# Optimization experiments

Hardware: AMD Instinct MI355X
Metric: run time of the kernel (lower is better)

## Reference

```python
import jax, jax.numpy as jnp
import numpy as np

B, N, C = 8, 4096, 1024
H = 16
D = C // H  # head_dim = 64
SCALE = D ** -0.5


def setup_inputs() -> dict:
    key = jax.random.key(0)
    ks = jax.random.split(key, 5)
    s = 0.02
    return {
        "x": jax.random.normal(ks[0], (B, N, C), dtype=jnp.float32),
        "Wq": jax.random.normal(ks[1], (C, C), dtype=jnp.float32) * s,
        "Wk": jax.random.normal(ks[2], (C, C), dtype=jnp.float32) * s,
        "Wv": jax.random.normal(ks[3], (C, C), dtype=jnp.float32) * s,
        "Wp": jax.random.normal(ks[4], (C, C), dtype=jnp.float32) * s,
        "bp": jnp.zeros((C,), dtype=jnp.float32),
    }


def reference(x, Wq, Wk, Wv, Wp, bp):
    b, n, c = x.shape
    # nn.Linear: y = x @ W^T (no bias for q/k/v)
    def split_heads(y):
        # (B,N,C) -> (B,N,H,D) -> permute(0,2,3,1) -> (B,H,D,N)
        return jnp.transpose(y.reshape(b, n, H, D), (0, 2, 3, 1))

    q = split_heads(x @ Wq.T)  # (B,H,D,N)
    k = split_heads(x @ Wk.T)  # (B,H,D,N)
    v = split_heads(x @ Wv.T)  # (B,H,D,N)

    # attn over head_dim (faithful to source layout): (B,H,D,D)
    attn = jnp.einsum('bhdn,bhen->bhde', q, k) * SCALE
    attn = jax.nn.softmax(attn, axis=-1)
    # (B,H,D,D) @ (B,H,D,N) -> (B,H,D,N); transpose(1,2) -> (B,D,H,N); reshape (B,N,C)
    out = jnp.einsum('bhde,bhen->bhdn', attn, v)
    out = jnp.transpose(out, (0, 2, 1, 3)).reshape(b, n, c)
    return out @ Wp.T + bp
```

## Files before the change

kernel.cpp:

```cpp
#include <hip/hip_runtime.h>


typedef __attribute__((ext_vector_type(4))) float f32x4;
typedef __attribute__((ext_vector_type(8))) _Float16 f16x8;
typedef __attribute__((ext_vector_type(4))) unsigned short u16x4;

__device__ __forceinline__ unsigned short f2h(float f) {
  union { _Float16 h; unsigned short u; } v;
  v.h = (_Float16)f;
  return v.u;
}

__global__ void cvt_f32_f16(const float* __restrict__ in, unsigned short* __restrict__ out, int n) {
  int i = (blockIdx.x * blockDim.x + threadIdx.x) * 4;
  if (i >= n) return;
  float4 v = *(const float4*)(in + i);
  u16x4 o;
  o.x = f2h(v.x); o.y = f2h(v.y); o.z = f2h(v.z); o.w = f2h(v.w);
  *(u16x4*)(out + i) = o;
}

#define LDS_LD 68
enum { EPI_F16_N = 0, EPI_F16_T = 1, EPI_F32_BIAS = 2 };

template <int EPI>
__global__ __launch_bounds__(256, 2) void gemm_bt(const unsigned short* __restrict__ A,
                                                  const unsigned short* __restrict__ Bt,
                                                  void* __restrict__ Cv,
                                                  const float* __restrict__ bias,
                                                  const int M, const int N, const int K) {
  __shared__ unsigned short lds[4 * 64 * LDS_LD];
  const int tid = threadIdx.x;
  const int wave = tid >> 6, lane = tid & 63;
  const int quad = lane >> 4, l15 = lane & 15;
  const int m0 = blockIdx.y * 128, n0 = blockIdx.x * 128;
  const int mb = (wave & 1) * 64, nb = (wave >> 1) * 64;

  const int sr = lane >> 2;
  const int sc = (lane & 3) ^ ((sr >> 1) & 3);

  const int swz = quad ^ ((l15 >> 1) & 3);
  int a_off[4], b_off[4];
#pragma unroll
  for (int t = 0; t < 4; t++) {
    a_off[t] = ((mb >> 4) + t) * 512 + (l15 * 4 + swz) * 8;
    b_off[t] = 4096 + ((nb >> 4) + t) * 512 + (l15 * 4 + swz) * 8;
  }

  const unsigned short* Ag = A + (size_t)(m0 + sr) * K + sc * 8;
  const unsigned short* Bg = Bt + (size_t)(n0 + sr) * K + sc * 8;

  f32x4 acc[4][4];
#pragma unroll
  for (int i = 0; i < 4; i++)
#pragma unroll
    for (int j = 0; j < 4; j++) acc[i][j] = f32x4{0.f, 0.f, 0.f, 0.f};

  for (int k0 = 0; k0 < K; k0 += 32) {
    __syncthreads();
#pragma unroll
    for (int rd = 0; rd < 2; rd++) {
      const int ch = rd * 4 + wave;
      __builtin_amdgcn_global_load_lds(
          (const __attribute__((address_space(1))) void*)(Ag + (size_t)ch * 16 * K + k0),
          (__attribute__((address_space(3))) void*)&lds[ch * 512], 16, 0, 0);
      __builtin_amdgcn_global_load_lds(
          (const __attribute__((address_space(1))) void*)(Bg + (size_t)ch * 16 * K + k0),
          (__attribute__((address_space(3))) void*)&lds[4096 + ch * 512], 16, 0, 0);
    }
    __syncthreads();

    f16x8 af[4], bf[4];
#pragma unroll
    for (int t = 0; t < 4; t++) {
      af[t] = *(const f16x8*)&lds[a_off[t]];
      bf[t] = *(const f16x8*)&lds[b_off[t]];
    }
#pragma unroll
    for (int mi = 0; mi < 4; mi++)
#pragma unroll
      for (int ni = 0; ni < 4; ni++)
        acc[mi][ni] = __builtin_amdgcn_mfma_f32_16x16x32_f16(af[mi], bf[ni], acc[mi][ni], 0, 0, 0);
  }

  __syncthreads();

  if (EPI == EPI_F32_BIAS) {
    float* C = (float*)Cv;
#pragma unroll
    for (int ni = 0; ni < 4; ni++) {
      const int col = n0 + nb + ni * 16 + l15;
      const float bv = bias[col];
#pragma unroll
      for (int mi = 0; mi < 4; mi++)
#pragma unroll
        for (int rr = 0; rr < 4; rr++) {
          const int row = m0 + mb + mi * 16 + quad * 4 + rr;
          C[(size_t)row * N + col] = acc[mi][ni][rr] + bv;
        }
    }
  } else {
    unsigned short* C = (unsigned short*)Cv;
    unsigned short* w = &lds[wave * 64 * LDS_LD];
#pragma unroll
    for (int mi = 0; mi < 4; mi++)
#pragma unroll
      for (int ni = 0; ni < 4; ni++)
#pragma unroll
        for (int rr = 0; rr < 4; rr++) {
          const int rl = mi * 16 + quad * 4 + rr;
          const int cl = ni * 16 + l15;
          if (EPI == EPI_F16_N)
            w[rl * LDS_LD + cl] = f2h(acc[mi][ni][rr]);
          else
            w[cl * LDS_LD + rl] = f2h(acc[mi][ni][rr]);
        }
#pragma unroll
    for (int p = 0; p < 8; p++) {
      const int a = p * 8 + (lane >> 3);
      const int b8 = (lane & 7) * 8;
      u16x4 lo = *(const u16x4*)&w[a * LDS_LD + b8];
      u16x4 hi = *(const u16x4*)&w[a * LDS_LD + b8 + 4];
      size_t gi;
      if (EPI == EPI_F16_N)
        gi = (size_t)(m0 + mb + a) * N + (n0 + nb + b8);
      else
        gi = (size_t)(n0 + nb + a) * M + (m0 + mb + b8);
      *(u16x4*)&C[gi] = lo;
      *(u16x4*)&C[gi + 4] = hi;
    }
  }
}

__global__ __launch_bounds__(256) void attn_fused(const unsigned short* __restrict__ qkt,
                                                  const unsigned short* __restrict__ vbuf,
                                                  unsigned short* __restrict__ y) {
  __shared__ unsigned short Ps[64 * 72];
  const int h = blockIdx.x, b = blockIdx.y, ns = blockIdx.z;
  const int tid = threadIdx.x;
  const int wave = tid >> 6, lane = tid & 63;
  const int quad = lane >> 4, l15 = lane & 15;

  f32x4 acc[4];
#pragma unroll
  for (int t = 0; t < 4; t++) acc[t] = f32x4{0.f, 0.f, 0.f, 0.f};

  const unsigned short* qp = qkt + (size_t)(h * 64 + wave * 16 + l15) * 32768 + b * 4096 + quad * 8;
  const unsigned short* kp[4];
#pragma unroll
  for (int et = 0; et < 4; et++)
    kp[et] = qkt + (size_t)(1024 + h * 64 + et * 16 + l15) * 32768 + b * 4096 + quad * 8;

#pragma unroll 4
  for (int k0 = 0; k0 < 4096; k0 += 32) {
    f16x8 aq = *(const f16x8*)(qp + k0);
#pragma unroll
    for (int et = 0; et < 4; et++) {
      f16x8 bk = *(const f16x8*)(kp[et] + k0);
      acc[et] = __builtin_amdgcn_mfma_f32_16x16x32_f16(aq, bk, acc[et], 0, 0, 0);
    }
  }

#pragma unroll
  for (int et = 0; et < 4; et++) acc[et] *= 0.125f;

#pragma unroll
  for (int rr = 0; rr < 4; rr++) {
    float m = fmaxf(fmaxf(acc[0][rr], acc[1][rr]), fmaxf(acc[2][rr], acc[3][rr]));
#pragma unroll
    for (int o = 1; o < 16; o <<= 1) m = fmaxf(m, __shfl_xor(m, o, 16));
    float s = 0.f;
#pragma unroll
    for (int et = 0; et < 4; et++) {
      float p = __expf(acc[et][rr] - m);
      acc[et][rr] = p;
      s += p;
    }
#pragma unroll
    for (int o = 1; o < 16; o <<= 1) s += __shfl_xor(s, o, 16);
    const float inv = 1.f / s;
    const int drow = wave * 16 + quad * 4 + rr;
#pragma unroll
    for (int et = 0; et < 4; et++)
      Ps[drow * 72 + et * 16 + l15] = f2h(acc[et][rr] * inv);
  }

  __syncthreads();

  f16x8 pa0 = *(const f16x8*)&Ps[(wave * 16 + l15) * 72 + quad * 8];
  f16x8 pa1 = *(const f16x8*)&Ps[(wave * 16 + l15) * 72 + 32 + quad * 8];

  const unsigned short* vb =
      vbuf + (size_t)(b * 4096 + ns * 2048 + l15) * 1024 + h * 64 + quad * 8;
  unsigned short* yb = y + (size_t)b * (4096 * 1024);

  for (int nt = 0; nt < 128; nt++) {
    const unsigned short* vp = vb + (size_t)nt * 16 * 1024;
    f16x8 v0 = *(const f16x8*)(vp);
    f16x8 v1 = *(const f16x8*)(vp + 32);
    f32x4 o = f32x4{0.f, 0.f, 0.f, 0.f};
    o = __builtin_amdgcn_mfma_f32_16x16x32_f16(pa0, v0, o, 0, 0, 0);
    o = __builtin_amdgcn_mfma_f32_16x16x32_f16(pa1, v1, o, 0, 0, 0);
    const int n = ns * 2048 + nt * 16 + l15;
    const int nhi = n >> 10, nlo = n & 1023;
#pragma unroll
    for (int rr = 0; rr < 4; rr++) {
      const int d = wave * 16 + quad * 4 + rr;
      yb[(size_t)(d * 64 + h * 4 + nhi) * 1024 + nlo] = f2h(o[rr]);
    }
  }
}

extern "C" void kernel_launch(void* const* d_in, const int* in_sizes, int n_in, void* d_out,
                              int out_size, void* d_ws, size_t ws_size, hipStream_t stream) {
  (void)in_sizes; (void)n_in; (void)out_size; (void)ws_size;
  const float* x = (const float*)d_in[0];
  const float* Wq = (const float*)d_in[1];
  const float* Wk = (const float*)d_in[2];
  const float* Wv = (const float*)d_in[3];
  const float* Wp = (const float*)d_in[4];
  const float* bp = (const float*)d_in[5];

  char* ws = (char*)d_ws;
  unsigned short* xb = (unsigned short*)(ws);
  unsigned short* yb = xb;
  unsigned short* qkt = (unsigned short*)(ws + (size_t)67108864);
  unsigned short* vb = (unsigned short*)(ws + (size_t)201326592);
  unsigned short* wqk = (unsigned short*)(ws + (size_t)268435456);
  unsigned short* wv = (unsigned short*)(ws + (size_t)272629760);
  unsigned short* wp = (unsigned short*)(ws + (size_t)274726912);

  cvt_f32_f16<<<32768, 256, 0, stream>>>(x, xb, 33554432);
  cvt_f32_f16<<<1024, 256, 0, stream>>>(Wq, wqk, 1048576);
  cvt_f32_f16<<<1024, 256, 0, stream>>>(Wk, wqk + 1048576, 1048576);
  cvt_f32_f16<<<1024, 256, 0, stream>>>(Wv, wv, 1048576);
  cvt_f32_f16<<<1024, 256, 0, stream>>>(Wp, wp, 1048576);

  gemm_bt<EPI_F16_T><<<dim3(16, 256), 256, 0, stream>>>(xb, wqk, qkt, nullptr, 32768, 2048, 1024);
  gemm_bt<EPI_F16_N><<<dim3(8, 256), 256, 0, stream>>>(xb, wv, vb, nullptr, 32768, 1024, 1024);
  attn_fused<<<dim3(16, 8, 2), 256, 0, stream>>>(qkt, vb, yb);
  gemm_bt<EPI_F32_BIAS><<<dim3(8, 256), 256, 0, stream>>>(yb, wp, (float*)d_out, bp, 32768, 1024, 1024);
}
```

Before: 733.4 us.

## Split attention into split-K logits, softmax and PV kernels; fuse QKV GEMM

The old fused attention kernel used only a few hundred blocks, and each computed the full 4096-long QK^T reduction serially, redundantly per N-half. The new code splits it into three kernels. A logits kernel does split-K over 8 chunks and writes fp32 partials, a softmax kernel sums the partials and normalises, and a PV kernel uses 8-way N splitting. The Q, K and V projections are merged into one GEMM whose epilogue picks transposed or normal layout by column block, and the four weight conversions are merged into one launch. The cost is extra launches and an fp32 partial buffer round trip through memory, with workspace regions reused carefully.

New measurement: 697.1 us. -4.9%, faster.

```diff
diff --git a/kernel.cpp b/kernel.cpp
--- a/kernel.cpp
+++ b/kernel.cpp
@@ -20,8 +20,26 @@
   *(u16x4*)(out + i) = o;
 }
 
+__global__ void cvt4_f32_f16(const float* __restrict__ s0, const float* __restrict__ s1,
+                             const float* __restrict__ s2, const float* __restrict__ s3,
+                             unsigned short* __restrict__ d0, unsigned short* __restrict__ d1,
+                             unsigned short* __restrict__ d2, unsigned short* __restrict__ d3) {
+  const float* src; unsigned short* dst;
+  switch (blockIdx.y) {
+    case 0: src = s0; dst = d0; break;
+    case 1: src = s1; dst = d1; break;
+    case 2: src = s2; dst = d2; break;
+    default: src = s3; dst = d3; break;
+  }
+  int i = (blockIdx.x * blockDim.x + threadIdx.x) * 4;
+  float4 v = *(const float4*)(src + i);
+  u16x4 o;
+  o.x = f2h(v.x); o.y = f2h(v.y); o.z = f2h(v.z); o.w = f2h(v.w);
+  *(u16x4*)(dst + i) = o;
+}
+
 #define LDS_LD 68
-enum { EPI_F16_N = 0, EPI_F16_T = 1, EPI_F32_BIAS = 2 };
+enum { EPI_QKV = 0, EPI_F32_BIAS = 2 };
 
 template <int EPI>
 __global__ __launch_bounds__(256, 2) void gemm_bt(const unsigned short* __restrict__ A,
@@ -101,6 +119,7 @@
     }
   } else {
     unsigned short* C = (unsigned short*)Cv;
+    const bool isT = (n0 < 2048);
     unsigned short* w = &lds[wave * 64 * LDS_LD];
 #pragma unroll
     for (int mi = 0; mi < 4; mi++)
@@ -110,10 +129,10 @@
         for (int rr = 0; rr < 4; rr++) {
           const int rl = mi * 16 + quad * 4 + rr;
           const int cl = ni * 16 + l15;
-          if (EPI == EPI_F16_N)
+          if (isT)
+            w[cl * LDS_LD + rl] = f2h(acc[mi][ni][rr]);
+          else
             w[rl * LDS_LD + cl] = f2h(acc[mi][ni][rr]);
-          else
-            w[cl * LDS_LD + rl] = f2h(acc[mi][ni][rr]);
         }
 #pragma unroll
     for (int p = 0; p < 8; p++) {
@@ -122,21 +141,19 @@
       u16x4 lo = *(const u16x4*)&w[a * LDS_LD + b8];
       u16x4 hi = *(const u16x4*)&w[a * LDS_LD + b8 + 4];
       size_t gi;
-      if (EPI == EPI_F16_N)
-        gi = (size_t)(m0 + mb + a) * N + (n0 + nb + b8);
+      if (isT)
+        gi = (size_t)(n0 + nb + a) * M + (m0 + mb + b8);
       else
-        gi = (size_t)(n0 + nb + a) * M + (m0 + mb + b8);
+        gi = (size_t)2048 * 32768 + (size_t)(m0 + mb + a) * 1024 + (n0 - 2048 + nb + b8);
       *(u16x4*)&C[gi] = lo;
       *(u16x4*)&C[gi + 4] = hi;
     }
   }
 }
 
-__global__ __launch_bounds__(256) void attn_fused(const unsigned short* __restrict__ qkt,
-                                                  const unsigned short* __restrict__ vbuf,
-                                                  unsigned short* __restrict__ y) {
-  __shared__ unsigned short Ps[64 * 72];
-  const int h = blockIdx.x, b = blockIdx.y, ns = blockIdx.z;
+__global__ __launch_bounds__(256) void attn_logits(const unsigned short* __restrict__ qkt,
+                                                   float* __restrict__ pbuf) {
+  const int h = blockIdx.x, b = blockIdx.y, s = blockIdx.z;
   const int tid = threadIdx.x;
   const int wave = tid >> 6, lane = tid & 63;
   const int quad = lane >> 4, l15 = lane & 15;
@@ -145,14 +162,15 @@
 #pragma unroll
   for (int t = 0; t < 4; t++) acc[t] = f32x4{0.f, 0.f, 0.f, 0.f};
 
-  const unsigned short* qp = qkt + (size_t)(h * 64 + wave * 16 + l15) * 32768 + b * 4096 + quad * 8;
+  const unsigned short* qp =
+      qkt + (size_t)(h * 64 + wave * 16 + l15) * 32768 + b * 4096 + s * 512 + quad * 8;
   const unsigned short* kp[4];
 #pragma unroll
   for (int et = 0; et < 4; et++)
-    kp[et] = qkt + (size_t)(1024 + h * 64 + et * 16 + l15) * 32768 + b * 4096 + quad * 8;
+    kp[et] = qkt + (size_t)(1024 + h * 64 + et * 16 + l15) * 32768 + b * 4096 + s * 512 + quad * 8;
 
 #pragma unroll 4
-  for (int k0 = 0; k0 < 4096; k0 += 32) {
+  for (int k0 = 0; k0 < 512; k0 += 32) {
     f16x8 aq = *(const f16x8*)(qp + k0);
 #pragma unroll
     for (int et = 0; et < 4; et++) {
@@ -161,47 +179,86 @@
     }
   }
 
-#pragma unroll
-  for (int et = 0; et < 4; et++) acc[et] *= 0.125f;
-
-#pragma unroll
-  for (int rr = 0; rr < 4; rr++) {
-    float m = fmaxf(fmaxf(acc[0][rr], acc[1][rr]), fmaxf(acc[2][rr], acc[3][rr]));
-#pragma unroll
-    for (int o = 1; o < 16; o <<= 1) m = fmaxf(m, __shfl_xor(m, o, 16));
-    float s = 0.f;
-#pragma unroll
-    for (int et = 0; et < 4; et++) {
-      float p = __expf(acc[et][rr] - m);
-      acc[et][rr] = p;
-      s += p;
-    }
-#pragma unroll
-    for (int o = 1; o < 16; o <<= 1) s += __shfl_xor(s, o, 16);
-    const float inv = 1.f / s;
-    const int drow = wave * 16 + quad * 4 + rr;
-#pragma unroll
-    for (int et = 0; et < 4; et++)
-      Ps[drow * 72 + et * 16 + l15] = f2h(acc[et][rr] * inv);
-  }
-
-  __syncthreads();
-
-  f16x8 pa0 = *(const f16x8*)&Ps[(wave * 16 + l15) * 72 + quad * 8];
-  f16x8 pa1 = *(const f16x8*)&Ps[(wave * 16 + l15) * 72 + 32 + quad * 8];
+  float* pb = pbuf + ((size_t)(b * 16 + h) * 8 + s) * 4096;
+#pragma unroll
+  for (int et = 0; et < 4; et++)
+#pragma unroll
+    for (int rr = 0; rr < 4; rr++)
+      pb[(wave * 16 + quad * 4 + rr) * 64 + et * 16 + l15] = acc[et][rr];
+}
+
+__global__ __launch_bounds__(256) void attn_softmax(const float* __restrict__ pbuf,
+                                                    unsigned short* __restrict__ pP) {
+  const int bh = blockIdx.x;
+  const int tid = threadIdx.x;
+  const int d = tid >> 2, q4 = tid & 3;
+  const float* pb = pbuf + (size_t)bh * 32768 + d * 64 + q4 * 16;
+
+  float v[16];
+#pragma unroll
+  for (int i = 0; i < 16; i++) v[i] = 0.f;
+  for (int s = 0; s < 8; s++) {
+#pragma unroll
+    for (int e4 = 0; e4 < 4; e4++) {
+      float4 t = *(const float4*)(pb + s * 4096 + e4 * 4);
+      v[e4 * 4 + 0] += t.x; v[e4 * 4 + 1] += t.y;
+      v[e4 * 4 + 2] += t.z; v[e4 * 4 + 3] += t.w;
+    }
+  }
+#pragma unroll
+  for (int i = 0; i < 16; i++) v[i] *= 0.125f;
+
+  float m = v[0];
+#pragma unroll
+  for (int i = 1; i < 16; i++) m = fmaxf(m, v[i]);
+  m = fmaxf(m, __shfl_xor(m, 1));
+  m = fmaxf(m, __shfl_xor(m, 2));
+  float sum = 0.f;
+#pragma unroll
+  for (int i = 0; i < 16; i++) {
+    v[i] = __expf(v[i] - m);
+    sum += v[i];
+  }
+  sum += __shfl_xor(sum, 1);
+  sum += __shfl_xor(sum, 2);
+  const float inv = 1.f / sum;
+
+  unsigned short* pp = pP + (size_t)bh * 4096 + d * 64 + q4 * 16;
+#pragma unroll
+  for (int e4 = 0; e4 < 4; e4++) {
+    u16x4 o;
+    o.x = f2h(v[e4 * 4 + 0] * inv); o.y = f2h(v[e4 * 4 + 1] * inv);
+    o.z = f2h(v[e4 * 4 + 2] * inv); o.w = f2h(v[e4 * 4 + 3] * inv);
+    *(u16x4*)(pp + e4 * 4) = o;
+  }
+}
+
+__global__ __launch_bounds__(256) void attn_pv(const unsigned short* __restrict__ pP,
+                                               const unsigned short* __restrict__ vbuf,
+                                               unsigned short* __restrict__ y) {
+  const int h = blockIdx.x, b = blockIdx.y, s = blockIdx.z;
+  const int tid = threadIdx.x;
+  const int wave = tid >> 6, lane = tid & 63;
+  const int quad = lane >> 4, l15 = lane & 15;
+  const int bh = b * 16 + h;
+
+  const unsigned short* pp = pP + (size_t)bh * 4096 + (wave * 16 + l15) * 64 + quad * 8;
+  f16x8 pa0 = *(const f16x8*)(pp);
+  f16x8 pa1 = *(const f16x8*)(pp + 32);
 
   const unsigned short* vb =
-      vbuf + (size_t)(b * 4096 + ns * 2048 + l15) * 1024 + h * 64 + quad * 8;
+      vbuf + (size_t)(b * 4096 + s * 512 + l15) * 1024 + h * 64 + quad * 8;
   unsigned short* yb = y + (size_t)b * (4096 * 1024);
 
-  for (int nt = 0; nt < 128; nt++) {
+#pragma unroll 4
+  for (int nt = 0; nt < 32; nt++) {
     const unsigned short* vp = vb + (size_t)nt * 16 * 1024;
     f16x8 v0 = *(const f16x8*)(vp);
     f16x8 v1 = *(const f16x8*)(vp + 32);
     f32x4 o = f32x4{0.f, 0.f, 0.f, 0.f};
     o = __builtin_amdgcn_mfma_f32_16x16x32_f16(pa0, v0, o, 0, 0, 0);
     o = __builtin_amdgcn_mfma_f32_16x16x32_f16(pa1, v1, o, 0, 0, 0);
-    const int n = ns * 2048 + nt * 16 + l15;
+    const int n = s * 512 + nt * 16 + l15;
     const int nhi = n >> 10, nlo = n & 1023;
 #pragma unroll
     for (int rr = 0; rr < 4; rr++) {
@@ -223,21 +280,23 @@
 
   char* ws = (char*)d_ws;
   unsigned short* xb = (unsigned short*)(ws);
+  float* pbuf = (float*)(ws);
   unsigned short* yb = xb;
   unsigned short* qkt = (unsigned short*)(ws + (size_t)67108864);
-  unsigned short* vb = (unsigned short*)(ws + (size_t)201326592);
-  unsigned short* wqk = (unsigned short*)(ws + (size_t)268435456);
-  unsigned short* wv = (unsigned short*)(ws + (size_t)272629760);
+  unsigned short* pP = qkt;
+  unsigned short* vbuf = (unsigned short*)(ws + (size_t)201326592);
+  unsigned short* wqkv = (unsigned short*)(ws + (size_t)268435456);
   unsigned short* wp = (unsigned short*)(ws + (size_t)274726912);
 
   cvt_f32_f16<<<32768, 256, 0, stream>>>(x, xb, 33554432);
-  cvt_f32_f16<<<1024, 256, 0, stream>>>(Wq, wqk, 1048576);
-  cvt_f32_f16<<<1024, 256, 0, stream>>>(Wk, wqk + 1048576, 1048576);
-  cvt_f32_f16<<<1024, 256, 0, stream>>>(Wv, wv, 1048576);
-  cvt_f32_f16<<<1024, 256, 0, stream>>>(Wp, wp, 1048576);
-
-  gemm_bt<EPI_F16_T><<<dim3(16, 256), 256, 0, stream>>>(xb, wqk, qkt, nullptr, 32768, 2048, 1024);
-  gemm_bt<EPI_F16_N><<<dim3(8, 256), 256, 0, stream>>>(xb, wv, vb, nullptr, 32768, 1024, 1024);
-  attn_fused<<<dim3(16, 8, 2), 256, 0, stream>>>(qkt, vb, yb);
+  cvt4_f32_f16<<<dim3(1024, 4), 256, 0, stream>>>(Wq, Wk, Wv, Wp, wqkv, wqkv + 1048576,
+                                                  wqkv + 2097152, wp);
+
+  gemm_bt<EPI_QKV><<<dim3(24, 256), 256, 0, stream>>>(xb, wqkv, qkt, nullptr, 32768, 3072, 1024);
+
+  attn_logits<<<dim3(16, 8, 8), 256, 0, stream>>>(qkt, pbuf);
+  attn_softmax<<<128, 256, 0, stream>>>(pbuf, pP);
+  attn_pv<<<dim3(16, 8, 8), 256, 0, stream>>>(pP, vbuf, yb);
+
   gemm_bt<EPI_F32_BIAS><<<dim3(8, 256), 256, 0, stream>>>(yb, wp, (float*)d_out, bp, 32768, 1024, 1024);
 }
```
